# Performance work log

Measured on AMD Instinct MI355X. Metric: run time of the kernel, lower is better.

## Reference

```python
import jax, jax.numpy as jnp
import numpy as np

BN_EPS = 1e-5


def _gin_layer(h, src, dst, w1, b1, w2, b2, gamma, beta):
    n = h.shape[0]
    # GINConv, eps=0: MLP(x + sum_{j->i} x_j); messages gathered at src, scattered to dst
    agg = jax.ops.segment_sum(h[src], dst, num_segments=n)
    h = agg + h
    h = jnp.maximum(h @ w1 + b1, 0.0) @ w2 + b2
    h = jnp.maximum(h, 0.0)  # F.relu after conv
    # BatchNorm1d, training-mode batch statistics (biased var)
    mean = h.mean(axis=0)
    var = h.var(axis=0)
    return (h - mean) * jax.lax.rsqrt(var + BN_EPS) * gamma + beta


def setup_inputs() -> dict:
    key = jax.random.key(0)
    ks = jax.random.split(key, 32)
    N, E, F_IN, DIM, L, G = 100000, 1600000, 128, 64, 3, 1000
    inp = {
        "x": jax.random.normal(ks[0], (N, F_IN), dtype=jnp.float32),
        "edge_index": jax.random.randint(ks[1], (2, E), 0, N, dtype=jnp.int64),
        "batch": jnp.sort(jax.random.randint(ks[2], (N,), 0, G, dtype=jnp.int64)),
        "num_graphs": G,
    }
    k = 3
    for i in range(L):
        din = F_IN if i == 0 else DIM
        inp[f"l{i}_w1"] = jax.random.normal(ks[k], (din, DIM), dtype=jnp.float32) * 0.05; k += 1
        inp[f"l{i}_b1"] = jnp.zeros((DIM,), dtype=jnp.float32)
        inp[f"l{i}_w2"] = jax.random.normal(ks[k], (DIM, DIM), dtype=jnp.float32) * 0.05; k += 1
        inp[f"l{i}_b2"] = jnp.zeros((DIM,), dtype=jnp.float32)
        inp[f"l{i}_gamma"] = jnp.ones((DIM,), dtype=jnp.float32)
        inp[f"l{i}_beta"] = jnp.zeros((DIM,), dtype=jnp.float32)
    return inp


def reference(x, edge_index, batch, num_graphs,
              l0_w1, l0_b1, l0_w2, l0_b2, l0_gamma, l0_beta,
              l1_w1, l1_b1, l1_w2, l1_b2, l1_gamma, l1_beta,
              l2_w1, l2_b1, l2_w2, l2_b2, l2_gamma, l2_beta):
    src, dst = edge_index[0], edge_index[1]
    params = [
        (l0_w1, l0_b1, l0_w2, l0_b2, l0_gamma, l0_beta),
        (l1_w1, l1_b1, l1_w2, l1_b2, l1_gamma, l1_beta),
        (l2_w1, l2_b1, l2_w2, l2_b2, l2_gamma, l2_beta),
    ]
    h = x
    xs = []
    for p in params:
        h = _gin_layer(h, src, dst, *p)
        xs.append(h)
    # global_add_pool per layer, then concat along features
    xpool = [jax.ops.segment_sum(h, batch, num_segments=num_graphs) for h in xs]
    return jnp.concatenate(xpool, axis=1), jnp.concatenate(xs, axis=1)
```

## Files before the change

kernel.cpp:

```cpp
#include <hip/hip_runtime.h>

#define DIM 64
#define XS_STRIDE 192
#define BN_EPS 1e-5f
#define B_MAX 512
#define P4_CAP 6144
#define CSR_CHUNK 16384
#define BSPACE 1280

__device__ inline unsigned pack_bf16x2(float lo, float hi) {
    unsigned ulo = __float_as_uint(lo); ulo = (ulo + 0x7FFFu + ((ulo >> 16) & 1u)) >> 16;
    unsigned uhi = __float_as_uint(hi); uhi = (uhi + 0x7FFFu + ((uhi >> 16) & 1u)) >> 16;
    return ulo | (uhi << 16);
}
__device__ inline float2 unpack_bf16x2(unsigned v) {
    return make_float2(__uint_as_float(v << 16), __uint_as_float(v & 0xFFFF0000u));
}

__global__ void setup_kernel(float* __restrict__ stats, unsigned* __restrict__ ybf, int N) {
    int t = threadIdx.x;
    if (t < 3 * 256) stats[t] = 0.f;
    if (t < 32) ybf[(size_t)N * 32 + t] = 0u;
}

__global__ __launch_bounds__(256) void p1_hist(const int* __restrict__ dsts, long long E,
                                               int NB1, int B, int* __restrict__ bh) {
    __shared__ int hist[B_MAX];
    const int i = blockIdx.x, t = threadIdx.x;
    for (int b = t; b < B; b += 256) hist[b] = 0;
    __syncthreads();
    long long s0 = (long long)i * CSR_CHUNK;
    long long s1 = s0 + CSR_CHUNK; if (s1 > E) s1 = E;
    for (long long e = s0 + t; e < s1; e += 256)
        atomicAdd(&hist[dsts[e] >> 8], 1);
    __syncthreads();
    for (int b = t; b < B; b += 256) bh[b * NB1 + i] = hist[b];
}

__global__ __launch_bounds__(1024) void p2_scan(int* __restrict__ bh, int total_n) {
    __shared__ int sbuf[2][1024];
    const int t = threadIdx.x;
    const int seg = (total_n + 1023) / 1024;
    int s0 = t * seg, s1 = s0 + seg; if (s1 > total_n) s1 = total_n;
    int s = 0;
    for (int i = s0; i < s1; i++) s += bh[i];
    sbuf[0][t] = s; __syncthreads();
    int c = 0;
    for (int o = 1; o < 1024; o <<= 1) {
        int val = sbuf[c][t];
        if (t >= o) val += sbuf[c][t - o];
        sbuf[c ^ 1][t] = val; __syncthreads(); c ^= 1;
    }
    int run = sbuf[c][t] - s;
    for (int i = s0; i < s1; i++) { int v = bh[i]; bh[i] = run; run += v; }
}

__global__ __launch_bounds__(256) void p3_part(const int* __restrict__ edges, long long E,
                                               int NB1, int B, const int* __restrict__ bh,
                                               unsigned* __restrict__ ebuf) {
    __shared__ int cur[B_MAX];
    const int i = blockIdx.x, t = threadIdx.x;
    for (int b = t; b < B; b += 256) cur[b] = bh[b * NB1 + i];
    __syncthreads();
    long long s0 = (long long)i * CSR_CHUNK;
    long long s1 = s0 + CSR_CHUNK; if (s1 > E) s1 = E;
    for (long long e = s0 + t; e < s1; e += 256) {
        int src = edges[e];
        int dst = edges[E + e];
        int b = dst >> 8;
        int pos = atomicAdd(&cur[b], 1);
        ebuf[pos] = (unsigned)src | ((unsigned)(dst & 255) << 24);
    }
}

__global__ __launch_bounds__(256) void p4_build(const unsigned* __restrict__ ebuf, long long E,
                                                int NB1, int B, const int* __restrict__ bh,
                                                int* __restrict__ offsets, int* __restrict__ psz,
                                                int* __restrict__ eidx, int N) {
    __shared__ unsigned lbuf[P4_CAP];
    __shared__ int hist[256];
    __shared__ int sbuf[2][256];
    __shared__ int cur[256];
    __shared__ int lstart[256];
    const int b = blockIdx.x, t = threadIdx.x;
    const int s = bh[b * NB1];
    const int e = (b + 1 < B) ? bh[(b + 1) * NB1] : (int)E;
    const int sz = e - s;
    const int ps = ((s + 3) & ~3) + b * BSPACE;
    const int next_raw = (b + 1 < B) ? bh[(b + 1) * NB1] : (int)E;
    const int next_ps = ((next_raw + 3) & ~3) + (b + 1) * BSPACE;
    const bool inl = (sz <= P4_CAP);
    if (inl) for (int k = t; k < sz; k += 256) lbuf[k] = ebuf[s + k];
    hist[t] = 0;
    __syncthreads();
    for (int k = t; k < sz; k += 256) {
        unsigned v = inl ? lbuf[k] : ebuf[s + k];
        atomicAdd(&hist[v >> 24], 1);
    }
    __syncthreads();
    const int deg = hist[t];
    const int pad = max(4, (deg + 3) & ~3);
    sbuf[0][t] = pad; __syncthreads();
    int c = 0;
    for (int o = 1; o < 256; o <<= 1) {
        int val = sbuf[c][t];
        if (t >= o) val += sbuf[c][t - o];
        sbuf[c ^ 1][t] = val; __syncthreads(); c ^= 1;
    }
    const int excl = sbuf[c][t] - pad;
    const int total = sbuf[c][255];
    const int node = b * 256 + t;
    if (node < N) { offsets[node] = ps + excl; psz[node] = pad; }
    lstart[t] = excl;
    cur[t] = 0;
    __syncthreads();
    for (int k = t; k < sz; k += 256) {
        unsigned v = inl ? lbuf[k] : ebuf[s + k];
        int dl = v >> 24;
        int pos = atomicAdd(&cur[dl], 1);
        eidx[ps + lstart[dl] + pos] = (int)(v & 0xFFFFFFu);
    }
    for (int k = deg; k < pad; k++) eidx[ps + excl + k] = N;
    __syncthreads();
    for (int i = ps + total + t; i < next_ps; i += 256) eidx[i] = N;
}

template<int DIN, bool FUSE>
__global__ __launch_bounds__(256) void proj_kernel(
    const float* __restrict__ h, int h_stride, int h_off,
    float* __restrict__ h_back,
    const float* __restrict__ w1,
    const float* __restrict__ stats_prev,
    const float* __restrict__ gamma_prev, const float* __restrict__ beta_prev,
    unsigned* __restrict__ ybf, int N)
{
    constexpr int R = 32;
    __shared__ float w1s[DIN * DIM];
    __shared__ float hin[R][DIN];
    __shared__ float scshs[2 * DIM];
    const int tid = threadIdx.x;
    const int row0 = blockIdx.x * R;

    if (FUSE && tid < DIM) {
        float inv_n = 1.0f / (float)N;
        float mean = stats_prev[tid] * inv_n;
        float var  = stats_prev[DIM + tid] * inv_n - mean * mean;
        float sc   = gamma_prev[tid] * rsqrtf(var + BN_EPS);
        scshs[tid] = sc;
        scshs[DIM + tid] = beta_prev[tid] - mean * sc;
    }
    for (int i = tid; i < DIN * DIM / 4; i += 256)
        *(float4*)&w1s[i * 4] = *(const float4*)&w1[i * 4];
    if (FUSE) __syncthreads();
    for (int i = tid; i < R * DIN / 4; i += 256) {
        int r = i / (DIN / 4), k4 = (i % (DIN / 4)) * 4;
        int row = row0 + r;
        float4 hv = make_float4(0.f, 0.f, 0.f, 0.f);
        if (row < N) {
            hv = *(const float4*)&h[(size_t)row * h_stride + h_off + k4];
            if (FUSE) {
                hv.x = hv.x * scshs[k4 + 0] + scshs[DIM + k4 + 0];
                hv.y = hv.y * scshs[k4 + 1] + scshs[DIM + k4 + 1];
                hv.z = hv.z * scshs[k4 + 2] + scshs[DIM + k4 + 2];
                hv.w = hv.w * scshs[k4 + 3] + scshs[DIM + k4 + 3];
                *(float4*)&h_back[(size_t)row * h_stride + h_off + k4] = hv;
            }
        }
        *(float4*)&hin[r][k4] = hv;
    }
    __syncthreads();

    const int hw = tid >> 5;
    const int hl = tid & 31;
    float a0[4], a1[4];
    #pragma unroll
    for (int q = 0; q < 4; q++) { a0[q] = 0.f; a1[q] = 0.f; }
    for (int k = 0; k < DIN; k++) {
        float w0 = w1s[k * DIM + 2 * hl];
        float w1v = w1s[k * DIM + 2 * hl + 1];
        #pragma unroll
        for (int q = 0; q < 4; q++) {
            float hv = hin[hw * 4 + q][k];
            a0[q] += hv * w0; a1[q] += hv * w1v;
        }
    }
    #pragma unroll
    for (int q = 0; q < 4; q++) {
        int row = row0 + hw * 4 + q;
        if (row < N) ybf[(size_t)row * 32 + hl] = pack_bf16x2(a0[q], a1[q]);
    }
}

__global__ __launch_bounds__(256) void aggmlp_kernel(
    const unsigned* __restrict__ ybf,
    const int* __restrict__ offsets, const int* __restrict__ psz,
    const int* __restrict__ eidx,
    const float* __restrict__ b1,
    const float* __restrict__ w2, const float* __restrict__ b2,
    float* __restrict__ xs, int xs_off,
    float* __restrict__ stats, int N)
{
    constexpr int R = 64;
    __shared__ float zin[R][DIM];
    __shared__ float sred[2][DIM];
    const int tid  = threadIdx.x;
    const int row0 = blockIdx.x * R;
    const int qw = tid >> 4;
    const int ql = tid & 15;
    const uint2* __restrict__ ybf2 = (const uint2*)ybf;

    if (tid < DIM) { sred[0][tid] = 0.f; sred[1][tid] = 0.f; }

    const float4 b1v = *(const float4*)&b1[ql * 4];
    int p0[4], sz[4];
    float ac[4][4];
    #pragma unroll
    for (int q = 0; q < 4; q++) {
        int node = row0 + qw * 4 + q;
        if (node < N) {
            p0[q] = offsets[node];
            sz[q] = psz[node];
            uint2 sv = ybf2[(size_t)node * 16 + ql];
            float2 lo = unpack_bf16x2(sv.x), hi = unpack_bf16x2(sv.y);
            ac[q][0] = lo.x + b1v.x; ac[q][1] = lo.y + b1v.y;
            ac[q][2] = hi.x + b1v.z; ac[q][3] = hi.y + b1v.w;
        } else {
            p0[q] = 0; sz[q] = 0;
            ac[q][0] = ac[q][1] = ac[q][2] = ac[q][3] = 0.f;
        }
    }
    int steps = 0;
    #pragma unroll
    for (int q = 0; q < 4; q++) steps = max(steps, sz[q] >> 2);

    int4 e4[4];
    #pragma unroll
    for (int q = 0; q < 4; q++)
        e4[q] = *(const int4*)&eidx[p0[q]];

    for (int s = 0; s < steps; s++) {
        const int b4 = 4 * s;
        uint2 g[4][4];
        #pragma unroll
        for (int q = 0; q < 4; q++) {
            g[q][0] = ybf2[(size_t)e4[q].x * 16 + ql];
            g[q][1] = ybf2[(size_t)e4[q].y * 16 + ql];
            g[q][2] = ybf2[(size_t)e4[q].z * 16 + ql];
            g[q][3] = ybf2[(size_t)e4[q].w * 16 + ql];
        }
        int4 e4n[4];
        #pragma unroll
        for (int q = 0; q < 4; q++) {
            int off = max(0, min(b4 + 4, sz[q] - 4));
            e4n[q] = *(const int4*)&eidx[p0[q] + off];
        }
        #pragma unroll
        for (int q = 0; q < 4; q++) {
            const float m = (b4 < sz[q]) ? 1.f : 0.f;
            #pragma unroll
            for (int j = 0; j < 4; j++) {
                float2 lo = unpack_bf16x2(g[q][j].x), hi = unpack_bf16x2(g[q][j].y);
                ac[q][0] += lo.x * m; ac[q][1] += lo.y * m;
                ac[q][2] += hi.x * m; ac[q][3] += hi.y * m;
            }
        }
        #pragma unroll
        for (int q = 0; q < 4; q++) e4[q] = e4n[q];
    }
    #pragma unroll
    for (int q = 0; q < 4; q++) {
        int r = qw * 4 + q;
        float4 z;
        z.x = fmaxf(ac[q][0], 0.f); z.y = fmaxf(ac[q][1], 0.f);
        z.z = fmaxf(ac[q][2], 0.f); z.w = fmaxf(ac[q][3], 0.f);
        *(float4*)&zin[r][ql * 4] = z;
    }
    __syncthreads();

    const int lane = tid & 63;
    const int wv_  = tid >> 6;
    float oacc[16];
    #pragma unroll
    for (int i = 0; i < 16; i++) oacc[i] = b2[lane];
    for (int k = 0; k < DIM; k++) {
        float w = w2[k * DIM + lane];
        #pragma unroll
        for (int i = 0; i < 16; i++) oacc[i] += zin[wv_ + 4 * i][k] * w;
    }
    float s1 = 0.f, s2 = 0.f;
    #pragma unroll
    for (int i = 0; i < 16; i++) {
        int row = row0 + wv_ + 4 * i;
        if (row < N) {
            float v = fmaxf(oacc[i], 0.f);
            xs[(size_t)row * XS_STRIDE + xs_off + lane] = v;
            s1 += v; s2 += v * v;
        }
    }
    atomicAdd(&sred[0][lane], s1);
    atomicAdd(&sred[1][lane], s2);
    __syncthreads();
    if (tid < DIM) {
        atomicAdd(&stats[tid], sred[0][tid]);
        atomicAdd(&stats[DIM + tid], sred[1][tid]);
    }
}

__global__ void pool_kernel(float* __restrict__ xs, const int* __restrict__ batch,
                            float* __restrict__ pool,
                            const float* __restrict__ stats2,
                            const float* __restrict__ gamma2, const float* __restrict__ beta2,
                            int N) {
    int g = blockIdx.x;
    int tid = threadIdx.x;
    float sc = 1.f, sh = 0.f;
    if (tid >= 2 * DIM) {
        int c = tid - 2 * DIM;
        float inv_n = 1.0f / (float)N;
        float mean = stats2[c] * inv_n;
        float var  = stats2[DIM + c] * inv_n - mean * mean;
        sc = gamma2[c] * rsqrtf(var + BN_EPS);
        sh = beta2[c] - mean * sc;
    }
    int lo = 0, hi = N;
    while (lo < hi) { int mid = (lo + hi) >> 1; if (batch[mid] < g) lo = mid + 1; else hi = mid; }
    int start = lo;
    hi = N;
    while (lo < hi) { int mid = (lo + hi) >> 1; if (batch[mid] < g + 1) lo = mid + 1; else hi = mid; }
    int end = lo;
    float s = 0.f;
    if (tid < 2 * DIM) {
        for (int n = start; n < end; n++) s += xs[(size_t)n * XS_STRIDE + tid];
    } else {
        for (int n = start; n < end; n++) {
            size_t p = (size_t)n * XS_STRIDE + tid;
            float v = xs[p] * sc + sh;
            xs[p] = v;
            s += v;
        }
    }
    pool[(size_t)g * XS_STRIDE + tid] = s;
}

extern "C" void kernel_launch(void* const* d_in, const int* in_sizes, int n_in,
                              void* d_out, int out_size, void* d_ws, size_t ws_size,
                              hipStream_t stream) {
    const float* x     = (const float*)d_in[0];
    const int*   edges = (const int*)d_in[1];
    const int*   batch = (const int*)d_in[2];

    const int  N    = in_sizes[2];
    const long long E = in_sizes[1] / 2;
    const int  F_IN = in_sizes[0] / N;
    const int  G    = out_size / XS_STRIDE - N;

    const float* W[3][6];
    for (int l = 0; l < 3; l++)
        for (int p = 0; p < 6; p++)
            W[l][p] = (const float*)d_in[4 + l * 6 + p];

    float* out_pool = (float*)d_out;
    float* out_xs   = out_pool + (size_t)G * XS_STRIDE;

    const int B   = (N + 255) >> 8;
    const int NB1 = (int)((E + CSR_CHUNK - 1) / CSR_CHUNK);
    const int EPAD = (int)(((E + 3) & ~3LL) + (long long)B * BSPACE + 64);

    unsigned* ybf  = (unsigned*)d_ws;
    float* stats   = (float*)(ybf + (size_t)(N + 1) * 32);
    int*   offsets = (int*)(stats + 3 * 256);
    int*   psz     = offsets + N + 1;
    int*   eidx    = psz + N;
    unsigned* ebuf = (unsigned*)(eidx + EPAD);
    int*   bh      = (int*)(ebuf + E);

    const int pblocks = (N + 31) / 32;
    const int ablocks = (N + 63) / 64;

    setup_kernel<<<1, 1024, 0, stream>>>(stats, ybf, N);
    p1_hist<<<NB1, 256, 0, stream>>>(edges + E, E, NB1, B, bh);
    p2_scan<<<1, 1024, 0, stream>>>(bh, B * NB1);
    p3_part<<<NB1, 256, 0, stream>>>(edges, E, NB1, B, bh, ebuf);
    p4_build<<<B, 256, 0, stream>>>(ebuf, E, NB1, B, bh, offsets, psz, eidx, N);

    for (int l = 0; l < 3; l++) {
        const int h_off = (l == 0) ? 0 : (l - 1) * DIM;
        float* statsL = stats + l * 256;

        if (l == 0)
            proj_kernel<128, false><<<pblocks, 256, 0, stream>>>(
                x, F_IN, 0, nullptr, W[l][0], nullptr, nullptr, nullptr, ybf, N);
        else
            proj_kernel<64, true><<<pblocks, 256, 0, stream>>>(
                out_xs, XS_STRIDE, h_off, out_xs, W[l][0],
                stats + (l - 1) * 256, W[l - 1][4], W[l - 1][5], ybf, N);

        aggmlp_kernel<<<ablocks, 256, 0, stream>>>(ybf, offsets, psz, eidx,
            W[l][1], W[l][2], W[l][3], out_xs, l * DIM, statsL, N);
    }

    pool_kernel<<<G, XS_STRIDE, 0, stream>>>(out_xs, batch, out_pool,
                                             stats + 2 * 256, W[2][4], W[2][5], N);
}
```

Baseline: 448.1 us.

## Merge setup into histogram, co-launch layer-0 projection with partition, overlap pooling

Removes the setup kernel by folding stats and ybf zeroing into block 0 of the histogram pass. Runs the layer-0 projection as extra blocks of the edge-partition kernel, and pools the first two layers' finished columns as extra blocks of the last aggregation kernel. This leaves a smaller final pool kernel that only normalises and sums the last layer. The aim is fewer launches and better GPU fill while the small serial CSR kernels run. The merged kernel needs more shared memory for the projection tiles, which may lower occupancy of the partition blocks.

```diff
diff --git a/kernel.cpp b/kernel.cpp
--- a/kernel.cpp
+++ b/kernel.cpp
@@ -17,16 +17,16 @@
     return make_float2(__uint_as_float(v << 16), __uint_as_float(v & 0xFFFF0000u));
 }
 
-__global__ void setup_kernel(float* __restrict__ stats, unsigned* __restrict__ ybf, int N) {
-    int t = threadIdx.x;
-    if (t < 3 * 256) stats[t] = 0.f;
-    if (t < 32) ybf[(size_t)N * 32 + t] = 0u;
-}
-
 __global__ __launch_bounds__(256) void p1_hist(const int* __restrict__ dsts, long long E,
-                                               int NB1, int B, int* __restrict__ bh) {
+                                               int NB1, int B, int* __restrict__ bh,
+                                               float* __restrict__ stats,
+                                               unsigned* __restrict__ ybf, int N) {
     __shared__ int hist[B_MAX];
     const int i = blockIdx.x, t = threadIdx.x;
+    if (i == 0) {
+        for (int k = t; k < 3 * 256; k += 256) stats[k] = 0.f;
+        if (t < 32) ybf[(size_t)N * 32 + t] = 0u;
+    }
     for (int b = t; b < B; b += 256) hist[b] = 0;
     __syncthreads();
     long long s0 = (long long)i * CSR_CHUNK;
@@ -55,21 +55,62 @@
     for (int i = s0; i < s1; i++) { int v = bh[i]; bh[i] = run; run += v; }
 }
 
-__global__ __launch_bounds__(256) void p3_part(const int* __restrict__ edges, long long E,
-                                               int NB1, int B, const int* __restrict__ bh,
-                                               unsigned* __restrict__ ebuf) {
+__global__ __launch_bounds__(256) void p3proj_kernel(
+    const int* __restrict__ edges, long long E, int NB1, int B,
+    const int* __restrict__ bh, unsigned* __restrict__ ebuf,
+    const float* __restrict__ x, int F_IN,
+    const float* __restrict__ w1, unsigned* __restrict__ ybf, int N)
+{
     __shared__ int cur[B_MAX];
-    const int i = blockIdx.x, t = threadIdx.x;
-    for (int b = t; b < B; b += 256) cur[b] = bh[b * NB1 + i];
-    __syncthreads();
-    long long s0 = (long long)i * CSR_CHUNK;
-    long long s1 = s0 + CSR_CHUNK; if (s1 > E) s1 = E;
-    for (long long e = s0 + t; e < s1; e += 256) {
-        int src = edges[e];
-        int dst = edges[E + e];
-        int b = dst >> 8;
-        int pos = atomicAdd(&cur[b], 1);
-        ebuf[pos] = (unsigned)src | ((unsigned)(dst & 255) << 24);
+    __shared__ float w1s[128 * DIM];
+    __shared__ float hin[32][128];
+    const int t = threadIdx.x;
+
+    if (blockIdx.x < NB1) {
+        const int i = blockIdx.x;
+        for (int b = t; b < B; b += 256) cur[b] = bh[b * NB1 + i];
+        __syncthreads();
+        long long s0 = (long long)i * CSR_CHUNK;
+        long long s1 = s0 + CSR_CHUNK; if (s1 > E) s1 = E;
+        for (long long e = s0 + t; e < s1; e += 256) {
+            int src = edges[e];
+            int dst = edges[E + e];
+            int b = dst >> 8;
+            int pos = atomicAdd(&cur[b], 1);
+            ebuf[pos] = (unsigned)src | ((unsigned)(dst & 255) << 24);
+        }
+        return;
+    }
+    const int row0 = (blockIdx.x - NB1) * 32;
+    for (int i = t; i < 128 * DIM / 4; i += 256)
+        *(float4*)&w1s[i * 4] = *(const float4*)&w1[i * 4];
+    for (int i = t; i < 32 * 128 / 4; i += 256) {
+        int r = i / 32, k4 = (i % 32) * 4;
+        int row = row0 + r;
+        float4 hv = make_float4(0.f, 0.f, 0.f, 0.f);
+        if (row < N) hv = *(const float4*)&x[(size_t)row * F_IN + k4];
+        *(float4*)&hin[r][k4] = hv;
+    }
+    __syncthreads();
+
+    const int hw = t >> 5;
+    const int hl = t & 31;
+    float a0[4], a1[4];
+    #pragma unroll
+    for (int q = 0; q < 4; q++) { a0[q] = 0.f; a1[q] = 0.f; }
+    for (int k = 0; k < 128; k++) {
+        float w0 = w1s[k * DIM + 2 * hl];
+        float w1v = w1s[k * DIM + 2 * hl + 1];
+        #pragma unroll
+        for (int q = 0; q < 4; q++) {
+            float hv = hin[hw * 4 + q][k];
+            a0[q] += hv * w0; a1[q] += hv * w1v;
+        }
+    }
+    #pragma unroll
+    for (int q = 0; q < 4; q++) {
+        int row = row0 + hw * 4 + q;
+        if (row < N) ybf[(size_t)row * 32 + hl] = pack_bf16x2(a0[q], a1[q]);
     }
 }
 
@@ -191,6 +232,7 @@
     }
 }
 
+template<bool WITH_POOL>
 __global__ __launch_bounds__(256) void aggmlp_kernel(
     const unsigned* __restrict__ ybf,
     const int* __restrict__ offsets, const int* __restrict__ psz,
@@ -198,12 +240,38 @@
     const float* __restrict__ b1,
     const float* __restrict__ w2, const float* __restrict__ b2,
     float* __restrict__ xs, int xs_off,
-    float* __restrict__ stats, int N)
+    float* __restrict__ stats, int N,
+    int ablocks, const int* __restrict__ batch, float* __restrict__ pool)
 {
     constexpr int R = 64;
     __shared__ float zin[R][DIM];
     __shared__ float sred[2][DIM];
     const int tid  = threadIdx.x;
+
+    if (WITH_POOL && blockIdx.x >= ablocks) {
+        const int g = blockIdx.x - ablocks;
+        const int half = tid >> 7, c = tid & 127;
+        int lo = 0, hi = N;
+        while (lo < hi) { int mid = (lo + hi) >> 1; if (batch[mid] < g) lo = mid + 1; else hi = mid; }
+        int start = lo;
+        hi = N;
+        while (lo < hi) { int mid = (lo + hi) >> 1; if (batch[mid] < g + 1) lo = mid + 1; else hi = mid; }
+        int end = lo;
+        int mid2 = (start + end) >> 1;
+        int rs = half ? mid2 : start;
+        int re = half ? end : mid2;
+        float s = 0.f;
+        for (int n = rs; n < re; n++) s += xs[(size_t)n * XS_STRIDE + c];
+        sred[half][c & 63] = 0.f;
+        zin[half][c & 63] = 0.f;
+        __syncthreads();
+        __shared__ float psum[2][128];
+        psum[half][c] = s;
+        __syncthreads();
+        if (half == 0) pool[(size_t)g * XS_STRIDE + c] = psum[0][c] + psum[1][c];
+        return;
+    }
+
     const int row0 = blockIdx.x * R;
     const int qw = tid >> 4;
     const int ql = tid & 15;
@@ -306,22 +374,18 @@
     }
 }
 
-__global__ void pool_kernel(float* __restrict__ xs, const int* __restrict__ batch,
-                            float* __restrict__ pool,
-                            const float* __restrict__ stats2,
-                            const float* __restrict__ gamma2, const float* __restrict__ beta2,
-                            int N) {
+__global__ void poolB_kernel(float* __restrict__ xs, const int* __restrict__ batch,
+                             float* __restrict__ pool,
+                             const float* __restrict__ stats2,
+                             const float* __restrict__ gamma2, const float* __restrict__ beta2,
+                             int N) {
     int g = blockIdx.x;
-    int tid = threadIdx.x;
-    float sc = 1.f, sh = 0.f;
-    if (tid >= 2 * DIM) {
-        int c = tid - 2 * DIM;
-        float inv_n = 1.0f / (float)N;
-        float mean = stats2[c] * inv_n;
-        float var  = stats2[DIM + c] * inv_n - mean * mean;
-        sc = gamma2[c] * rsqrtf(var + BN_EPS);
-        sh = beta2[c] - mean * sc;
-    }
+    int c = threadIdx.x;
+    float inv_n = 1.0f / (float)N;
+    float mean = stats2[c] * inv_n;
+    float var  = stats2[DIM + c] * inv_n - mean * mean;
+    float sc = gamma2[c] * rsqrtf(var + BN_EPS);
+    float sh = beta2[c] - mean * sc;
     int lo = 0, hi = N;
     while (lo < hi) { int mid = (lo + hi) >> 1; if (batch[mid] < g) lo = mid + 1; else hi = mid; }
     int start = lo;
@@ -329,17 +393,13 @@
     while (lo < hi) { int mid = (lo + hi) >> 1; if (batch[mid] < g + 1) lo = mid + 1; else hi = mid; }
     int end = lo;
     float s = 0.f;
-    if (tid < 2 * DIM) {
-        for (int n = start; n < end; n++) s += xs[(size_t)n * XS_STRIDE + tid];
-    } else {
-        for (int n = start; n < end; n++) {
-            size_t p = (size_t)n * XS_STRIDE + tid;
-            float v = xs[p] * sc + sh;
-            xs[p] = v;
-            s += v;
-        }
-    }
-    pool[(size_t)g * XS_STRIDE + tid] = s;
+    for (int n = start; n < end; n++) {
+        size_t p = (size_t)n * XS_STRIDE + 2 * DIM + c;
+        float v = xs[p] * sc + sh;
+        xs[p] = v;
+        s += v;
+    }
+    pool[(size_t)g * XS_STRIDE + 2 * DIM + c] = s;
 }
 
 extern "C" void kernel_launch(void* const* d_in, const int* in_sizes, int n_in,
@@ -377,28 +437,25 @@
     const int pblocks = (N + 31) / 32;
     const int ablocks = (N + 63) / 64;
 
-    setup_kernel<<<1, 1024, 0, stream>>>(stats, ybf, N);
-    p1_hist<<<NB1, 256, 0, stream>>>(edges + E, E, NB1, B, bh);
+    p1_hist<<<NB1, 256, 0, stream>>>(edges + E, E, NB1, B, bh, stats, ybf, N);
     p2_scan<<<1, 1024, 0, stream>>>(bh, B * NB1);
-    p3_part<<<NB1, 256, 0, stream>>>(edges, E, NB1, B, bh, ebuf);
+    p3proj_kernel<<<NB1 + pblocks, 256, 0, stream>>>(edges, E, NB1, B, bh, ebuf,
+                                                     x, F_IN, W[0][0], ybf, N);
     p4_build<<<B, 256, 0, stream>>>(ebuf, E, NB1, B, bh, offsets, psz, eidx, N);
 
-    for (int l = 0; l < 3; l++) {
-        const int h_off = (l == 0) ? 0 : (l - 1) * DIM;
-        float* statsL = stats + l * 256;
-
-        if (l == 0)
-            proj_kernel<128, false><<<pblocks, 256, 0, stream>>>(
-                x, F_IN, 0, nullptr, W[l][0], nullptr, nullptr, nullptr, ybf, N);
-        else
-            proj_kernel<64, true><<<pblocks, 256, 0, stream>>>(
-                out_xs, XS_STRIDE, h_off, out_xs, W[l][0],
-                stats + (l - 1) * 256, W[l - 1][4], W[l - 1][5], ybf, N);
-
-        aggmlp_kernel<<<ablocks, 256, 0, stream>>>(ybf, offsets, psz, eidx,
-            W[l][1], W[l][2], W[l][3], out_xs, l * DIM, statsL, N);
-    }
-
-    pool_kernel<<<G, XS_STRIDE, 0, stream>>>(out_xs, batch, out_pool,
-                                             stats + 2 * 256, W[2][4], W[2][5], N);
-}
+    aggmlp_kernel<false><<<ablocks, 256, 0, stream>>>(ybf, offsets, psz, eidx,
+        W[0][1], W[0][2], W[0][3], out_xs, 0, stats, N, ablocks, nullptr, nullptr);
+
+    proj_kernel<64, true><<<pblocks, 256, 0, stream>>>(
+        out_xs, XS_STRIDE, 0, out_xs, W[1][0], stats, W[0][4], W[0][5], ybf, N);
+    aggmlp_kernel<false><<<ablocks, 256, 0, stream>>>(ybf, offsets, psz, eidx,
+        W[1][1], W[1][2], W[1][3], out_xs, DIM, stats + 256, N, ablocks, nullptr, nullptr);
+
+    proj_kernel<64, true><<<pblocks, 256, 0, stream>>>(
+        out_xs, XS_STRIDE, DIM, out_xs, W[2][0], stats + 256, W[1][4], W[1][5], ybf, N);
+    aggmlp_kernel<true><<<ablocks + G, 256, 0, stream>>>(ybf, offsets, psz, eidx,
+        W[2][1], W[2][2], W[2][3], out_xs, 2 * DIM, stats + 512, N, ablocks, batch, out_pool);
+
+    poolB_kernel<<<G, DIM, 0, stream>>>(out_xs, batch, out_pool,
+                                        stats + 512, W[2][4], W[2][5], N);
+}
```

Result: faster. 434.5 us (-3.0%).
